# Kernel optimization log

Measured on AMD Instinct MI355X. Metric: run time of the kernel, lower is better.

The kernel has to match this reference:

```python
import jax, jax.numpy as jnp
import numpy as np

N_NODES = 100000
N_EDGES = 800000
HIDDEN = 128


def setup_inputs() -> dict:
    key = jax.random.key(0)
    k1, k2, k3, k4, k5, k6 = jax.random.split(key, 6)
    z = jax.random.normal(k1, (N_NODES, HIDDEN), dtype=jnp.float32)
    edge_index = jax.random.randint(k2, (2, N_EDGES), 0, N_NODES, dtype=jnp.int64)
    # nn.Linear params (torch default init scale ~ 1/sqrt(fan_in))
    s1 = 1.0 / np.sqrt(2 * HIDDEN)
    s2 = 1.0 / np.sqrt(HIDDEN)
    W1 = jax.random.uniform(k3, (2 * HIDDEN, HIDDEN), jnp.float32, -s1, s1)
    b1 = jax.random.uniform(k4, (HIDDEN,), jnp.float32, -s1, s1)
    W2 = jax.random.uniform(k5, (HIDDEN, 1), jnp.float32, -s2, s2)
    b2 = jax.random.uniform(k6, (1,), jnp.float32, -s2, s2)
    return {"z": z, "edge_index": edge_index, "W1": W1, "b1": b1, "W2": W2, "b2": b2}


def reference(z, edge_index, W1, b1, W2, b2):
    src, dst = edge_index[0], edge_index[1]
    # Gather endpoint features: [E, H] each. Avoid materializing the [E, 2H]
    # concat by splitting W1 into src/dst halves (same math as cat + matmul).
    W1_src, W1_dst = W1[:HIDDEN], W1[HIDDEN:]
    h = z[src] @ W1_src + z[dst] @ W1_dst + b1  # [E, H]
    h = jax.nn.relu(h)
    score = h @ W2 + b2  # [E, 1]
    return score
```

## Files before the change

kernel.cpp:

```cpp
#include <hip/hip_runtime.h>
#include <hip/hip_bf16.h>

#define N_NODES 100000
#define N_EDGES 800000
#define HIDDEN 128

typedef short frag_ab __attribute__((ext_vector_type(8)));
typedef float frag_cd __attribute__((ext_vector_type(4)));

__device__ inline unsigned short f2b(float f) {
    union { float f; unsigned u; } x; x.f = f;
    return (unsigned short)((x.u + 0x7fffu + ((x.u >> 16) & 1u)) >> 16);
}

__global__ __launch_bounds__(256) void transpose_w1(
    const float* __restrict__ W1, unsigned short* __restrict__ Bt)
{
    const int t  = threadIdx.x;
    const int nc = blockIdx.x * 4 + (t >> 6);
    const int k2 = (t & 63) * 2;
    const int col  = nc & 127;
    const int roff = (nc >= 128) ? 128 : 0;
    float f0 = W1[(size_t)(roff + k2)     * HIDDEN + col];
    float f1 = W1[(size_t)(roff + k2 + 1) * HIDDEN + col];
    unsigned pack = (unsigned)f2b(f0) | ((unsigned)f2b(f1) << 16);
    *(unsigned*)(Bt + (size_t)nc * HIDDEN + k2) = pack;
}

#define AS_STRIDE 136
#define CS_STRIDE 264

__global__ __launch_bounds__(256) void precompute_uv_mfma(
    const float* __restrict__ z, const unsigned short* __restrict__ Bt,
    const float* __restrict__ b1, unsigned short* __restrict__ UV)
{
    __shared__ unsigned short smem[64 * CS_STRIDE];
    const int t = threadIdx.x;
    const int m0 = blockIdx.x * 64;
    const int lane = t & 63;
    const int w = t >> 6;

    #pragma unroll
    for (int i = 0; i < 8; ++i) {
        int f4 = i * 256 + t;
        int m = f4 >> 5;
        int c4 = f4 & 31;
        float4 v = make_float4(0.f, 0.f, 0.f, 0.f);
        if (m0 + m < N_NODES)
            v = ((const float4*)z)[(size_t)(m0 + m) * 32 + c4];
        uint2 p;
        p.x = (unsigned)f2b(v.x) | ((unsigned)f2b(v.y) << 16);
        p.y = (unsigned)f2b(v.z) | ((unsigned)f2b(v.w) << 16);
        *(uint2*)&smem[m * AS_STRIDE + c4 * 4] = p;
    }

    const int wn = w * 64;
    const int g  = lane >> 4;
    const int lc = lane & 15;
    frag_ab b[4][4];
    #pragma unroll
    for (int nt = 0; nt < 4; ++nt) {
        const unsigned short* brow = Bt + (size_t)(wn + nt * 16 + lc) * HIDDEN;
        #pragma unroll
        for (int q = 0; q < 4; ++q)
            b[nt][q] = *(const frag_ab*)(brow + q * 32 + g * 8);
    }

    frag_cd acc[4][4];
    #pragma unroll
    for (int mt = 0; mt < 4; ++mt)
        #pragma unroll
        for (int nt = 0; nt < 4; ++nt)
            acc[mt][nt] = (frag_cd){0.f, 0.f, 0.f, 0.f};

    __syncthreads();

    #pragma unroll
    for (int q = 0; q < 4; ++q) {
        frag_ab a[4];
        #pragma unroll
        for (int mt = 0; mt < 4; ++mt)
            a[mt] = *(const frag_ab*)&smem[(mt * 16 + lc) * AS_STRIDE + q * 32 + g * 8];
        #pragma unroll
        for (int mt = 0; mt < 4; ++mt)
            #pragma unroll
            for (int nt = 0; nt < 4; ++nt)
                acc[mt][nt] = __builtin_amdgcn_mfma_f32_16x16x32_bf16(
                    a[mt], b[nt][q], acc[mt][nt], 0, 0, 0);
    }

    __syncthreads();

    #pragma unroll
    for (int nt = 0; nt < 4; ++nt) {
        int nc = wn + nt * 16 + lc;
        float bias = (nc < HIDDEN) ? b1[nc] : 0.f;
        #pragma unroll
        for (int mt = 0; mt < 4; ++mt)
            #pragma unroll
            for (int r = 0; r < 4; ++r)
                smem[(mt * 16 + g * 4 + r) * CS_STRIDE + nc] =
                    f2b(acc[mt][nt][r] + bias);
    }

    __syncthreads();

    #pragma unroll
    for (int i = 0; i < 8; ++i) {
        int f = i * 256 + t;
        int m = f >> 5;
        int c16 = f & 31;
        if (m0 + m < N_NODES) {
            uint4 val = *(const uint4*)&smem[m * CS_STRIDE + c16 * 8];
            *(uint4*)&UV[(size_t)(m0 + m) * 256 + c16 * 8] = val;
        }
    }
}

__device__ inline float2 bf2(unsigned u) {
    union { unsigned i; float f; } lo, hi;
    lo.i = u << 16;
    hi.i = u & 0xffff0000u;
    return make_float2(lo.f, hi.f);
}

__device__ inline float2 rfma2(unsigned u, unsigned v, float2 w, float2 acc) {
    float2 uf = bf2(u), vf = bf2(v);
    float2 s = make_float2(uf.x + vf.x, uf.y + vf.y);
    s.x = fmaxf(s.x, 0.f); s.y = fmaxf(s.y, 0.f);
    acc.x = __builtin_fmaf(s.x, w.x, acc.x);
    acc.y = __builtin_fmaf(s.y, w.y, acc.y);
    return acc;
}

__global__ __launch_bounds__(256) void edge_score(
    const int* __restrict__ ei, const unsigned short* __restrict__ UV,
    const float* __restrict__ W2, const float* __restrict__ B2,
    float* __restrict__ out)
{
    const int t = threadIdx.x;
    const int g = t & 7;
    const int e = blockIdx.x * 32 + (t >> 3);

    const float4* W24 = (const float4*)W2;
    const float4 w0 = W24[g * 4 + 0];
    const float4 w1 = W24[g * 4 + 1];
    const float4 w2 = W24[g * 4 + 2];
    const float4 w3 = W24[g * 4 + 3];

    float2 s2 = make_float2(0.f, 0.f);
    if (e < N_EDGES) {
        const int src = ei[e];
        const int dst = ei[N_EDGES + e];
        const uint4* up = (const uint4*)(UV + (size_t)src * 256) + g * 2;
        const uint4* vp = (const uint4*)(UV + (size_t)dst * 256 + 128) + g * 2;
        const uint4 ua = up[0];
        const uint4 ub = up[1];
        const uint4 va = vp[0];
        const uint4 vb = vp[1];

        s2 = rfma2(ua.x, va.x, make_float2(w0.x, w0.y), s2);
        s2 = rfma2(ua.y, va.y, make_float2(w0.z, w0.w), s2);
        s2 = rfma2(ua.z, va.z, make_float2(w1.x, w1.y), s2);
        s2 = rfma2(ua.w, va.w, make_float2(w1.z, w1.w), s2);
        s2 = rfma2(ub.x, vb.x, make_float2(w2.x, w2.y), s2);
        s2 = rfma2(ub.y, vb.y, make_float2(w2.z, w2.w), s2);
        s2 = rfma2(ub.z, vb.z, make_float2(w3.x, w3.y), s2);
        s2 = rfma2(ub.w, vb.w, make_float2(w3.z, w3.w), s2);
    }

    float sum = s2.x + s2.y;
    sum += __shfl_xor(sum, 1, 8);
    sum += __shfl_xor(sum, 2, 8);
    sum += __shfl_xor(sum, 4, 8);

    if (g == 0 && e < N_EDGES) out[e] = sum + B2[0];
}

extern "C" void kernel_launch(void* const* d_in, const int* in_sizes, int n_in,
                              void* d_out, int out_size, void* d_ws, size_t ws_size,
                              hipStream_t stream) {
    const float* z  = (const float*)d_in[0];
    const int*   ei = (const int*)d_in[1];
    const float* W1 = (const float*)d_in[2];
    const float* b1 = (const float*)d_in[3];
    const float* W2 = (const float*)d_in[4];
    const float* b2 = (const float*)d_in[5];
    float* out = (float*)d_out;

    unsigned short* UV = (unsigned short*)d_ws;
    unsigned short* Bt = UV + (size_t)N_NODES * 256;

    transpose_w1<<<64, 256, 0, stream>>>(W1, Bt);
    precompute_uv_mfma<<<(N_NODES + 63) / 64, 256, 0, stream>>>(z, Bt, b1, UV);
    edge_score<<<(N_EDGES + 31) / 32, 256, 0, stream>>>(ei, UV, W2, b2, out);
}
```

Measured before the change: 174.8 us.

## Persistent precompute kernel with z prefetch; two edges per thread group in scoring

The node precompute kernel becomes a persistent grid of 768 blocks that loops over 64-row tiles. B fragments and bias are loaded once per block, and the next tile's z rows are prefetched into registers while the current tile's MFMA and store run. A and C staging get separate LDS buffers. The edge scoring kernel now handles two edges per 8-lane group, which doubles the number of gathers in flight per thread and halves the grid. The costs are higher register pressure and bounds checks that depend on N_EDGES being divisible by 64.

```diff
diff --git a/kernel.cpp b/kernel.cpp
--- a/kernel.cpp
+++ b/kernel.cpp
@@ -4,6 +4,8 @@
 #define N_NODES 100000
 #define N_EDGES 800000
 #define HIDDEN 128
+#define N_TILES 1563
+#define PC_GRID 768
 
 typedef short frag_ab __attribute__((ext_vector_type(8)));
 typedef float frag_cd __attribute__((ext_vector_type(4)));
@@ -34,86 +36,109 @@
     const float* __restrict__ z, const unsigned short* __restrict__ Bt,
     const float* __restrict__ b1, unsigned short* __restrict__ UV)
 {
-    __shared__ unsigned short smem[64 * CS_STRIDE];
+    __shared__ unsigned short As[64 * AS_STRIDE];
+    __shared__ unsigned short Cs[64 * CS_STRIDE];
     const int t = threadIdx.x;
-    const int m0 = blockIdx.x * 64;
     const int lane = t & 63;
     const int w = t >> 6;
-
+    const int wn = w * 64;
+    const int g  = lane >> 4;
+    const int lc = lane & 15;
+
+    frag_ab b[4][4];
+    float bias[4];
+    #pragma unroll
+    for (int nt = 0; nt < 4; ++nt) {
+        int nc = wn + nt * 16 + lc;
+        bias[nt] = (nc < HIDDEN) ? b1[nc] : 0.f;
+        const unsigned short* brow = Bt + (size_t)nc * HIDDEN;
+        #pragma unroll
+        for (int q = 0; q < 4; ++q)
+            b[nt][q] = *(const frag_ab*)(brow + q * 32 + g * 8);
+    }
+
+    int tile = blockIdx.x;
+    float4 pf[8];
     #pragma unroll
     for (int i = 0; i < 8; ++i) {
         int f4 = i * 256 + t;
-        int m = f4 >> 5;
-        int c4 = f4 & 31;
-        float4 v = make_float4(0.f, 0.f, 0.f, 0.f);
-        if (m0 + m < N_NODES)
-            v = ((const float4*)z)[(size_t)(m0 + m) * 32 + c4];
-        uint2 p;
-        p.x = (unsigned)f2b(v.x) | ((unsigned)f2b(v.y) << 16);
-        p.y = (unsigned)f2b(v.z) | ((unsigned)f2b(v.w) << 16);
-        *(uint2*)&smem[m * AS_STRIDE + c4 * 4] = p;
-    }
-
-    const int wn = w * 64;
-    const int g  = lane >> 4;
-    const int lc = lane & 15;
-    frag_ab b[4][4];
-    #pragma unroll
-    for (int nt = 0; nt < 4; ++nt) {
-        const unsigned short* brow = Bt + (size_t)(wn + nt * 16 + lc) * HIDDEN;
-        #pragma unroll
-        for (int q = 0; q < 4; ++q)
-            b[nt][q] = *(const frag_ab*)(brow + q * 32 + g * 8);
-    }
-
-    frag_cd acc[4][4];
-    #pragma unroll
-    for (int mt = 0; mt < 4; ++mt)
-        #pragma unroll
-        for (int nt = 0; nt < 4; ++nt)
-            acc[mt][nt] = (frag_cd){0.f, 0.f, 0.f, 0.f};
-
-    __syncthreads();
-
-    #pragma unroll
-    for (int q = 0; q < 4; ++q) {
-        frag_ab a[4];
+        int m = tile * 64 + (f4 >> 5);
+        if (m >= N_NODES) m = N_NODES - 1;
+        pf[i] = ((const float4*)z)[(size_t)m * 32 + (f4 & 31)];
+    }
+
+    while (true) {
+        #pragma unroll
+        for (int i = 0; i < 8; ++i) {
+            int f4 = i * 256 + t;
+            int m = f4 >> 5;
+            int c4 = f4 & 31;
+            uint2 p;
+            p.x = (unsigned)f2b(pf[i].x) | ((unsigned)f2b(pf[i].y) << 16);
+            p.y = (unsigned)f2b(pf[i].z) | ((unsigned)f2b(pf[i].w) << 16);
+            *(uint2*)&As[m * AS_STRIDE + c4 * 4] = p;
+        }
+        __syncthreads();
+
+        const int next = tile + PC_GRID;
+        const bool have_next = (next < N_TILES);
+        if (have_next) {
+            #pragma unroll
+            for (int i = 0; i < 8; ++i) {
+                int f4 = i * 256 + t;
+                int m = next * 64 + (f4 >> 5);
+                if (m >= N_NODES) m = N_NODES - 1;
+                pf[i] = ((const float4*)z)[(size_t)m * 32 + (f4 & 31)];
+            }
+        }
+
+        frag_cd acc[4][4];
         #pragma unroll
         for (int mt = 0; mt < 4; ++mt)
-            a[mt] = *(const frag_ab*)&smem[(mt * 16 + lc) * AS_STRIDE + q * 32 + g * 8];
-        #pragma unroll
-        for (int mt = 0; mt < 4; ++mt)
             #pragma unroll
             for (int nt = 0; nt < 4; ++nt)
-                acc[mt][nt] = __builtin_amdgcn_mfma_f32_16x16x32_bf16(
-                    a[mt], b[nt][q], acc[mt][nt], 0, 0, 0);
-    }
-
-    __syncthreads();
-
-    #pragma unroll
-    for (int nt = 0; nt < 4; ++nt) {
-        int nc = wn + nt * 16 + lc;
-        float bias = (nc < HIDDEN) ? b1[nc] : 0.f;
-        #pragma unroll
-        for (int mt = 0; mt < 4; ++mt)
-            #pragma unroll
-            for (int r = 0; r < 4; ++r)
-                smem[(mt * 16 + g * 4 + r) * CS_STRIDE + nc] =
-                    f2b(acc[mt][nt][r] + bias);
-    }
-
-    __syncthreads();
-
-    #pragma unroll
-    for (int i = 0; i < 8; ++i) {
-        int f = i * 256 + t;
-        int m = f >> 5;
-        int c16 = f & 31;
-        if (m0 + m < N_NODES) {
-            uint4 val = *(const uint4*)&smem[m * CS_STRIDE + c16 * 8];
-            *(uint4*)&UV[(size_t)(m0 + m) * 256 + c16 * 8] = val;
-        }
+                acc[mt][nt] = (frag_cd){0.f, 0.f, 0.f, 0.f};
+        #pragma unroll
+        for (int q = 0; q < 4; ++q) {
+            frag_ab a[4];
+            #pragma unroll
+            for (int mt = 0; mt < 4; ++mt)
+                a[mt] = *(const frag_ab*)&As[(mt * 16 + lc) * AS_STRIDE + q * 32 + g * 8];
+            #pragma unroll
+            for (int mt = 0; mt < 4; ++mt)
+                #pragma unroll
+                for (int nt = 0; nt < 4; ++nt)
+                    acc[mt][nt] = __builtin_amdgcn_mfma_f32_16x16x32_bf16(
+                        a[mt], b[nt][q], acc[mt][nt], 0, 0, 0);
+        }
+        __syncthreads();
+
+        #pragma unroll
+        for (int nt = 0; nt < 4; ++nt) {
+            int nc = wn + nt * 16 + lc;
+            #pragma unroll
+            for (int mt = 0; mt < 4; ++mt)
+                #pragma unroll
+                for (int r = 0; r < 4; ++r)
+                    Cs[(mt * 16 + g * 4 + r) * CS_STRIDE + nc] =
+                        f2b(acc[mt][nt][r] + bias[nt]);
+        }
+        __syncthreads();
+
+        const int m0 = tile * 64;
+        #pragma unroll
+        for (int i = 0; i < 8; ++i) {
+            int f = i * 256 + t;
+            int m = f >> 5;
+            int c16 = f & 31;
+            if (m0 + m < N_NODES) {
+                uint4 val = *(const uint4*)&Cs[m * CS_STRIDE + c16 * 8];
+                *(uint4*)&UV[(size_t)(m0 + m) * 256 + c16 * 8] = val;
+            }
+        }
+        if (!have_next) break;
+        __syncthreads();
+        tile = next;
     }
 }
 
@@ -140,7 +165,9 @@
 {
     const int t = threadIdx.x;
     const int g = t & 7;
-    const int e = blockIdx.x * 32 + (t >> 3);
+    const int slot = t >> 3;
+    const int e0 = blockIdx.x * 64 + slot;
+    const int e1 = e0 + 32;
 
     const float4* W24 = (const float4*)W2;
     const float4 w0 = W24[g * 4 + 0];
@@ -148,33 +175,53 @@
     const float4 w2 = W24[g * 4 + 2];
     const float4 w3 = W24[g * 4 + 3];
 
-    float2 s2 = make_float2(0.f, 0.f);
-    if (e < N_EDGES) {
-        const int src = ei[e];
-        const int dst = ei[N_EDGES + e];
-        const uint4* up = (const uint4*)(UV + (size_t)src * 256) + g * 2;
-        const uint4* vp = (const uint4*)(UV + (size_t)dst * 256 + 128) + g * 2;
-        const uint4 ua = up[0];
-        const uint4 ub = up[1];
-        const uint4 va = vp[0];
-        const uint4 vb = vp[1];
-
-        s2 = rfma2(ua.x, va.x, make_float2(w0.x, w0.y), s2);
-        s2 = rfma2(ua.y, va.y, make_float2(w0.z, w0.w), s2);
-        s2 = rfma2(ua.z, va.z, make_float2(w1.x, w1.y), s2);
-        s2 = rfma2(ua.w, va.w, make_float2(w1.z, w1.w), s2);
-        s2 = rfma2(ub.x, vb.x, make_float2(w2.x, w2.y), s2);
-        s2 = rfma2(ub.y, vb.y, make_float2(w2.z, w2.w), s2);
-        s2 = rfma2(ub.z, vb.z, make_float2(w3.x, w3.y), s2);
-        s2 = rfma2(ub.w, vb.w, make_float2(w3.z, w3.w), s2);
-    }
-
-    float sum = s2.x + s2.y;
-    sum += __shfl_xor(sum, 1, 8);
-    sum += __shfl_xor(sum, 2, 8);
-    sum += __shfl_xor(sum, 4, 8);
-
-    if (g == 0 && e < N_EDGES) out[e] = sum + B2[0];
+    const int s0 = ei[e0];
+    const int d0 = ei[N_EDGES + e0];
+    const int s1 = ei[e1];
+    const int d1 = ei[N_EDGES + e1];
+
+    const uint4* u0p = (const uint4*)(UV + (size_t)s0 * 256) + g * 2;
+    const uint4* v0p = (const uint4*)(UV + (size_t)d0 * 256 + 128) + g * 2;
+    const uint4* u1p = (const uint4*)(UV + (size_t)s1 * 256) + g * 2;
+    const uint4* v1p = (const uint4*)(UV + (size_t)d1 * 256 + 128) + g * 2;
+    const uint4 ua0 = u0p[0], ub0 = u0p[1];
+    const uint4 va0 = v0p[0], vb0 = v0p[1];
+    const uint4 ua1 = u1p[0], ub1 = u1p[1];
+    const uint4 va1 = v1p[0], vb1 = v1p[1];
+
+    float2 A = make_float2(0.f, 0.f), B = make_float2(0.f, 0.f);
+    A = rfma2(ua0.x, va0.x, make_float2(w0.x, w0.y), A);
+    A = rfma2(ua0.y, va0.y, make_float2(w0.z, w0.w), A);
+    A = rfma2(ua0.z, va0.z, make_float2(w1.x, w1.y), A);
+    A = rfma2(ua0.w, va0.w, make_float2(w1.z, w1.w), A);
+    A = rfma2(ub0.x, vb0.x, make_float2(w2.x, w2.y), A);
+    A = rfma2(ub0.y, vb0.y, make_float2(w2.z, w2.w), A);
+    A = rfma2(ub0.z, vb0.z, make_float2(w3.x, w3.y), A);
+    A = rfma2(ub0.w, vb0.w, make_float2(w3.z, w3.w), A);
+
+    B = rfma2(ua1.x, va1.x, make_float2(w0.x, w0.y), B);
+    B = rfma2(ua1.y, va1.y, make_float2(w0.z, w0.w), B);
+    B = rfma2(ua1.z, va1.z, make_float2(w1.x, w1.y), B);
+    B = rfma2(ua1.w, va1.w, make_float2(w1.z, w1.w), B);
+    B = rfma2(ub1.x, vb1.x, make_float2(w2.x, w2.y), B);
+    B = rfma2(ub1.y, vb1.y, make_float2(w2.z, w2.w), B);
+    B = rfma2(ub1.z, vb1.z, make_float2(w3.x, w3.y), B);
+    B = rfma2(ub1.w, vb1.w, make_float2(w3.z, w3.w), B);
+
+    float sa = A.x + A.y;
+    float sb = B.x + B.y;
+    sa += __shfl_xor(sa, 1, 8);
+    sa += __shfl_xor(sa, 2, 8);
+    sa += __shfl_xor(sa, 4, 8);
+    sb += __shfl_xor(sb, 1, 8);
+    sb += __shfl_xor(sb, 2, 8);
+    sb += __shfl_xor(sb, 4, 8);
+
+    if (g == 0) {
+        float bb = B2[0];
+        out[e0] = sa + bb;
+        out[e1] = sb + bb;
+    }
 }
 
 extern "C" void kernel_launch(void* const* d_in, const int* in_sizes, int n_in,
@@ -192,6 +239,6 @@
     unsigned short* Bt = UV + (size_t)N_NODES * 256;
 
     transpose_w1<<<64, 256, 0, stream>>>(W1, Bt);
-    precompute_uv_mfma<<<(N_NODES + 63) / 64, 256, 0, stream>>>(z, Bt, b1, UV);
-    edge_score<<<(N_EDGES + 31) / 32, 256, 0, stream>>>(ei, UV, W2, b2, out);
-}
+    precompute_uv_mfma<<<PC_GRID, 256, 0, stream>>>(z, Bt, b1, UV);
+    edge_score<<<N_EDGES / 64, 256, 0, stream>>>(ei, UV, W2, b2, out);
+}
```

After: 166.0 us. 5.1% less time.
